# Kernel optimization log

Measured on AMD Instinct MI355X. Metric: run time of the kernel, lower is better.

## Reference

```python
import jax, jax.numpy as jnp
import numpy as np

B, T, E_DIM, H, J, V = 32, 1000, 512, 512, 512, 1024
BLANK = 0

def setup_inputs() -> dict:
    key = jax.random.key(0)
    ks = jax.random.split(key, 8)
    s = lambda k, shp, sc: jax.random.normal(k, shp, jnp.float32) * sc
    return {
        "encoder_output": jax.random.normal(ks[0], (B, T, E_DIM), jnp.float32),
        "embed": s(ks[1], (V, H), 0.02),
        "W_ih": s(ks[2], (H, 4 * H), 0.05),
        "W_hh": s(ks[3], (H, 4 * H), 0.05),
        "b_lstm": jnp.zeros((4 * H,), jnp.float32),
        "W_enc": s(ks[4], (E_DIM, J), 0.05),
        "W_dec": s(ks[5], (H, J), 0.05),
        "b_joint": jnp.zeros((J,), jnp.float32),
        "W_out": s(ks[6], (J, V), 0.05),
    }

def _lstm_step(tok, h, c, embed, W_ih, W_hh, b):
    # prediction network: embedding lookup + single-layer LSTM cell
    x = embed[tok]                                   # [B, H]
    gates = x @ W_ih + h @ W_hh + b                  # [B, 4H]
    i, f, g, o = jnp.split(gates, 4, axis=-1)
    c_new = jax.nn.sigmoid(f) * c + jax.nn.sigmoid(i) * jnp.tanh(g)
    h_new = jax.nn.sigmoid(o) * jnp.tanh(c_new)
    return h_new, c_new

def reference(encoder_output, embed, W_ih, W_hh, b_lstm, W_enc, W_dec, b_joint, W_out):
    # transducer_greedy_decode (beam_size <= 1 path), vectorized over batch,
    # sequential over encoder time steps via lax.scan.
    Bv = encoder_output.shape[0]
    h0 = jnp.zeros((Bv, H), encoder_output.dtype)
    c0 = jnp.zeros((Bv, H), encoder_output.dtype)
    tok0 = jnp.full((Bv,), BLANK, jnp.int32)
    # initial decoder call on blank token with zero hidden
    out_PN0, c1 = _lstm_step(tok0, h0, c0, embed, W_ih, W_hh, b_lstm)
    # precompute encoder projection of the joint (same math, one big GEMM)
    enc_proj = encoder_output @ W_enc                # [B, T, J]

    def step(carry, enc_t):
        out_PN, h, c, score = carry
        logits = jnp.tanh(enc_t + out_PN @ W_dec + b_joint) @ W_out   # [B, V]
        logp = jax.nn.log_softmax(logits, axis=-1)
        lp = jnp.max(logp, axis=-1)                  # best log-prob
        pos = jnp.argmax(logp, axis=-1)              # best token
        emit = pos != BLANK                          # hypotheses to update
        h_new, c_new = _lstm_step(pos.astype(jnp.int32), h, c, embed, W_ih, W_hh, b_lstm)
        m = emit[:, None]
        out_PN = jnp.where(m, h_new, out_PN)
        h = jnp.where(m, h_new, h)
        c = jnp.where(m, c_new, c)
        score = score + jnp.where(emit, lp, 0.0)
        tok = jnp.where(emit, pos, BLANK)            # BLANK marks 'no emission'
        return (out_PN, h, c, score), tok

    init = (out_PN0, out_PN0, c1, jnp.zeros((Bv,), encoder_output.dtype))
    (_, _, _, scores), toks = jax.lax.scan(step, init, jnp.swapaxes(enc_proj, 0, 1))
    predictions = toks.T                             # [B, T], BLANK = no emission
    mean_exp_score = jnp.exp(scores).mean()
    return predictions, scores, mean_exp_score
```

## Files before the change

### kernel.cpp

```cpp
#include <hip/hip_runtime.h>
#include <math.h>

#define BB 32
#define TT 1000
#define HH 512
#define JJ 512
#define VV 1024
#define G4 2048
#define NB 128
#define NT 1024

#define RLX __ATOMIC_RELAXED
#define AGT __HIP_MEMORY_SCOPE_AGENT

__device__ __align__(16) float g_encp[(size_t)TT * JJ * BB];
__device__ __align__(16) float g_E[(size_t)VV * G4];
__device__ __align__(16) float g_h[HH * BB];
__device__ __align__(16) float g_c[BB * HH];
__device__ __align__(16) float g_joint[JJ * BB];
__device__ __align__(16) float g_hW[BB * G4];
__device__ float g_pm[BB * NB];
__device__ float g_ps[BB * NB];
__device__ int   g_pa[BB * NB];
__device__ float g_score[BB];
__device__ int g_arr[3][NB];

__global__ __launch_bounds__(256) void k_encproj(const float* __restrict__ enc,
                                                 const float* __restrict__ Wenc) {
    __shared__ __align__(16) float x[BB * 512];
    const int t = blockIdx.x;
    for (int i = threadIdx.x; i < BB * 128; i += 256) {
        const int b = i >> 7, k4 = i & 127;
        *reinterpret_cast<float4*>(x + b * 512 + k4 * 4) =
            *reinterpret_cast<const float4*>(enc + ((size_t)(b * TT + t)) * 512 + k4 * 4);
    }
    __syncthreads();
    const int j = threadIdx.x;
    float acc0[BB], acc1[BB];
#pragma unroll
    for (int b = 0; b < BB; ++b) { acc0[b] = 0.f; acc1[b] = 0.f; }
    for (int k4 = 0; k4 < 128; ++k4) {
        const int k = k4 * 4;
        float w0[4], w1[4];
#pragma unroll
        for (int i = 0; i < 4; ++i) {
            w0[i] = Wenc[(size_t)(k + i) * JJ + j];
            w1[i] = Wenc[(size_t)(k + i) * JJ + j + 256];
        }
#pragma unroll
        for (int b = 0; b < BB; ++b) {
            const float4 xv = *reinterpret_cast<const float4*>(x + b * 512 + k);
            acc0[b] += xv.x * w0[0] + xv.y * w0[1] + xv.z * w0[2] + xv.w * w0[3];
            acc1[b] += xv.x * w1[0] + xv.y * w1[1] + xv.z * w1[2] + xv.w * w1[3];
        }
    }
    float* outt = g_encp + (size_t)t * JJ * BB;
#pragma unroll
    for (int b = 0; b < BB; ++b) {
        outt[j * BB + b]         = acc0[b];
        outt[(j + 256) * BB + b] = acc1[b];
    }
}

__global__ __launch_bounds__(256) void k_embproj(const float* __restrict__ emb,
                                                 const float* __restrict__ Wih) {
    __shared__ __align__(16) float x[BB * 512];
    const int v0 = (blockIdx.x >> 2) * 32;
    const int g0 = (blockIdx.x & 3) * 512;
    for (int i = threadIdx.x; i < BB * 128; i += 256) {
        const int b = i >> 7, k4 = i & 127;
        *reinterpret_cast<float4*>(x + b * 512 + k4 * 4) =
            *reinterpret_cast<const float4*>(emb + (size_t)(v0 + b) * 512 + k4 * 4);
    }
    __syncthreads();
    const int j = g0 + threadIdx.x;
    float acc0[BB], acc1[BB];
#pragma unroll
    for (int b = 0; b < BB; ++b) { acc0[b] = 0.f; acc1[b] = 0.f; }
    for (int k4 = 0; k4 < 128; ++k4) {
        const int k = k4 * 4;
        float w0[4], w1[4];
#pragma unroll
        for (int i = 0; i < 4; ++i) {
            w0[i] = Wih[(size_t)(k + i) * G4 + j];
            w1[i] = Wih[(size_t)(k + i) * G4 + j + 256];
        }
#pragma unroll
        for (int b = 0; b < BB; ++b) {
            const float4 xv = *reinterpret_cast<const float4*>(x + b * 512 + k);
            acc0[b] += xv.x * w0[0] + xv.y * w0[1] + xv.z * w0[2] + xv.w * w0[3];
            acc1[b] += xv.x * w1[0] + xv.y * w1[1] + xv.z * w1[2] + xv.w * w1[3];
        }
    }
#pragma unroll
    for (int b = 0; b < BB; ++b) {
        g_E[(size_t)(v0 + b) * G4 + j]       = acc0[b];
        g_E[(size_t)(v0 + b) * G4 + j + 256] = acc1[b];
    }
}

__global__ void k_init(const float* __restrict__ bl) {
    const int k = threadIdx.x;
    const float ig = g_E[k]        + bl[k];
    const float gg = g_E[1024 + k] + bl[1024 + k];
    const float og = g_E[1536 + k] + bl[1536 + k];
    const float si = 1.f / (1.f + expf(-ig));
    const float so = 1.f / (1.f + expf(-og));
    const float c1 = si * tanhf(gg);
    const float h1 = so * tanhf(c1);
    for (int b = 0; b < BB; ++b) {
        g_h[k * BB + b] = h1;
        g_c[b * HH + k] = c1;
    }
    if (k < BB) g_score[k] = 0.f;
    if (k < 3 * NB) ((int*)g_arr)[k] = 0;
}

template<int KN>
__device__ __forceinline__ void mv4(const float* __restrict__ w_lds, const int wpad,
                                    const int c0, const int k0,
                                    const float* __restrict__ x_lds,
                                    const int ks, const int b4, float acc[4][4]) {
#pragma unroll
    for (int c = 0; c < 4; ++c)
#pragma unroll
        for (int r = 0; r < 4; ++r) acc[c][r] = 0.f;
#pragma unroll 8
    for (int i = 0; i < KN; ++i) {
        const int k = k0 + i * 8 + ks;
        const float4 xv = *reinterpret_cast<const float4*>(x_lds + k * 32 + b4 * 4);
        const float4 wv = *reinterpret_cast<const float4*>(w_lds + k * wpad + c0);
        acc[0][0] += wv.x * xv.x; acc[0][1] += wv.x * xv.y; acc[0][2] += wv.x * xv.z; acc[0][3] += wv.x * xv.w;
        acc[1][0] += wv.y * xv.x; acc[1][1] += wv.y * xv.y; acc[1][2] += wv.y * xv.z; acc[1][3] += wv.y * xv.w;
        acc[2][0] += wv.z * xv.x; acc[2][1] += wv.z * xv.y; acc[2][2] += wv.z * xv.z; acc[2][3] += wv.z * xv.w;
        acc[3][0] += wv.w * xv.x; acc[3][1] += wv.w * xv.y; acc[3][2] += wv.w * xv.z; acc[3][3] += wv.w * xv.w;
    }
#pragma unroll
    for (int off = 8; off <= 32; off <<= 1)
#pragma unroll
        for (int c = 0; c < 4; ++c)
#pragma unroll
            for (int r = 0; r < 4; ++r) acc[c][r] += __shfl_xor(acc[c][r], off, 64);
}

__global__ __launch_bounds__(NT) void k_loop(const float* __restrict__ Wdec,
                                             const float* __restrict__ Wout,
                                             const float* __restrict__ Whh,
                                             const float* __restrict__ bj,
                                             const float* __restrict__ bl,
                                             float* __restrict__ out) {
    __shared__ __align__(16) float x_lds[512 * 32];
    __shared__ __align__(16) float wab_lds[512 * 20];
    __shared__ __align__(16) float wout_lds[512 * 12];
    __shared__ float part_lds[560];
    __shared__ float logit_lds[8 * 33];
    __shared__ float red_m[2], red_s[2];
    __shared__ int   red_a[2];
    __shared__ int   red_bar[2];
    __shared__ int   bar_done;

    const int blk = blockIdx.x, tid = threadIdx.x;
    const int wv = tid >> 6, lane = tid & 63, ks = lane >> 3, b4 = lane & 7;
    const int row = blk >> 2, qs = blk & 3;

    for (int i = tid; i < 512 * 20; i += NT) {
        const int k = i / 20, c = i - k * 20;
        wab_lds[i] = (c < 16) ? Whh[(size_t)k * G4 + blk * 16 + c]
                              : Wdec[(size_t)k * JJ + blk * 4 + (c - 16)];
    }
    for (int i = tid; i < 512 * 12; i += NT) {
        const int k = i / 12, c = i - k * 12;
        wout_lds[i] = (c < 8) ? Wout[(size_t)k * VV + blk * 8 + c] : 0.f;
    }
    float bjr[4];
#pragma unroll
    for (int c = 0; c < 4; ++c) bjr[c] = bj[blk * 4 + c];
    __syncthreads();

    float acc[4][4];
    for (int t = 0; t < TT; ++t) {
        const int tp1 = t + 1;
        {
            float v[16];
#pragma unroll
            for (int p = 0; p < 16; ++p)
                v[p] = __hip_atomic_load(&g_h[tid + p * 1024], RLX, AGT);
#pragma unroll
            for (int p = 0; p < 16; ++p) x_lds[tid + p * 1024] = v[p];
        }
        float encr[4];
        if (wv == 8 && lane < 32) {
            const float* ep = g_encp + (size_t)t * JJ * BB + (size_t)blk * 4 * BB;
#pragma unroll
            for (int c = 0; c < 4; ++c) encr[c] = ep[c * BB + lane];
        }
        __syncthreads();
        if (wv < 4) {
            mv4<64>(wab_lds, 20, wv * 4, 0, x_lds, ks, b4, acc);
            if (ks == 0) {
#pragma unroll
                for (int c = 0; c < 4; ++c)
#pragma unroll
                    for (int j = 0; j < 4; ++j)
                        __hip_atomic_store(&g_hW[(size_t)(b4 * 4 + j) * G4 + blk * 16 + wv * 4 + c],
                                           acc[c][j], RLX, AGT);
            }
        } else if (wv < 8) {
            mv4<16>(wab_lds, 20, 16, (wv - 4) * 128, x_lds, ks, b4, acc);
            if (ks == 0) {
#pragma unroll
                for (int c = 0; c < 4; ++c)
#pragma unroll
                    for (int j = 0; j < 4; ++j)
                        part_lds[(wv - 4) * 136 + c * 33 + b4 * 4 + j] = acc[c][j];
            }
        }
        __syncthreads();
        if (wv == 8 && lane < 32) {
            const int b = lane;
#pragma unroll
            for (int c = 0; c < 4; ++c) {
                const float u = part_lds[c * 33 + b] + part_lds[136 + c * 33 + b]
                              + part_lds[272 + c * 33 + b] + part_lds[408 + c * 33 + b]
                              + encr[c] + bjr[c];
                __hip_atomic_store(&g_joint[(blk * 4 + c) * BB + b], tanhf(u), RLX, AGT);
            }
        }
        __syncthreads();
        if (tid == 0) __hip_atomic_store(&g_arr[0][blk], tp1, RLX, AGT);
        for (;;) {
            int m = 0x7fffffff;
            if (tid < NB) m = __hip_atomic_load(&g_arr[0][tid], RLX, AGT);
#pragma unroll
            for (int off = 32; off; off >>= 1) m = min(m, __shfl_xor(m, off, 64));
            if (lane == 0 && wv < 2) red_bar[wv] = m;
            __syncthreads();
            if (tid == 0) bar_done = (min(red_bar[0], red_bar[1]) >= tp1);
            __syncthreads();
            if (bar_done) break;
            __builtin_amdgcn_s_sleep(1);
        }

        {
            float v[16];
#pragma unroll
            for (int p = 0; p < 16; ++p)
                v[p] = __hip_atomic_load(&g_joint[tid + p * 1024], RLX, AGT);
#pragma unroll
            for (int p = 0; p < 16; ++p) x_lds[tid + p * 1024] = v[p];
        }
        __syncthreads();
        if (wv < 4) {
            const int tile = wv & 1, kh = wv >> 1;
            mv4<32>(wout_lds, 12, tile * 4, kh * 256, x_lds, ks, b4, acc);
            if (kh == 1 && ks == 0) {
#pragma unroll
                for (int c = 0; c < 4; ++c)
#pragma unroll
                    for (int j = 0; j < 4; ++j)
                        part_lds[tile * 160 + c * 33 + b4 * 4 + j] = acc[c][j];
            }
        }
        __syncthreads();
        if (wv < 2 && ks == 0) {
#pragma unroll
            for (int c = 0; c < 4; ++c)
#pragma unroll
                for (int j = 0; j < 4; ++j)
                    logit_lds[(wv * 4 + c) * 33 + b4 * 4 + j] =
                        acc[c][j] + part_lds[wv * 160 + c * 33 + b4 * 4 + j];
        }
        __syncthreads();
        if (wv == 0 && lane < BB) {
            const int b = lane;
            float m = -1e30f; int a = 0;
#pragma unroll
            for (int c = 0; c < 8; ++c) {
                const float l = logit_lds[c * 33 + b];
                if (l > m) { m = l; a = blk * 8 + c; }
            }
            float s = 0.f;
#pragma unroll
            for (int c = 0; c < 8; ++c) s += expf(logit_lds[c * 33 + b] - m);
            __hip_atomic_store(&g_pm[b * NB + blk], m, RLX, AGT);
            __hip_atomic_store(&g_pa[b * NB + blk], a, RLX, AGT);
            __hip_atomic_store(&g_ps[b * NB + blk], s, RLX, AGT);
        }
        __syncthreads();
        if (tid == 0) __hip_atomic_store(&g_arr[1][blk], tp1, RLX, AGT);
        for (;;) {
            int m = 0x7fffffff;
            if (tid < NB) m = __hip_atomic_load(&g_arr[1][tid], RLX, AGT);
#pragma unroll
            for (int off = 32; off; off >>= 1) m = min(m, __shfl_xor(m, off, 64));
            if (lane == 0 && wv < 2) red_bar[wv] = m;
            __syncthreads();
            if (tid == 0) bar_done = (min(red_bar[0], red_bar[1]) >= tp1);
            __syncthreads();
            if (bar_done) break;
            __builtin_amdgcn_s_sleep(1);
        }

        {
            float m0 = -1e30f, s0 = 0.f; int a0 = 1 << 30;
            if (tid < NB) {
                m0 = __hip_atomic_load(&g_pm[row * NB + tid], RLX, AGT);
                a0 = __hip_atomic_load(&g_pa[row * NB + tid], RLX, AGT);
                s0 = __hip_atomic_load(&g_ps[row * NB + tid], RLX, AGT);
            }
            float m = m0; int a = a0;
#pragma unroll
            for (int off = 32; off; off >>= 1) {
                const float om = __shfl_xor(m, off, 64);
                const int   oa = __shfl_xor(a, off, 64);
                if (om > m || (om == m && oa < a)) { m = om; a = oa; }
            }
            if (lane == 0 && wv < 2) { red_m[wv] = m; red_a[wv] = a; }
            __syncthreads();
            float M; int P;
            {
                const float ma = red_m[0], mb = red_m[1];
                const int aa = red_a[0], ab = red_a[1];
                if (mb > ma || (mb == ma && ab < aa)) { M = mb; P = ab; }
                else { M = ma; P = aa; }
            }
            float e = (tid < NB) ? s0 * expf(m0 - M) : 0.f;
#pragma unroll
            for (int off = 32; off; off >>= 1) e += __shfl_xor(e, off, 64);
            if (lane == 0 && wv < 2) red_s[wv] = e;
            __syncthreads();
            if (qs == 0 && tid == 0) {
                out[row * TT + t] = (float)P;
                if (P != 0) g_score[row] += -logf(red_s[0] + red_s[1]);
            }
            if (P != 0 && tid < 128) {
                const int k = qs * 128 + tid;
                const float* Ep = g_E + (size_t)P * G4;
                const float hw0 = __hip_atomic_load(&g_hW[(size_t)row * G4 + k],        RLX, AGT);
                const float hw1 = __hip_atomic_load(&g_hW[(size_t)row * G4 + 512 + k],  RLX, AGT);
                const float hw2 = __hip_atomic_load(&g_hW[(size_t)row * G4 + 1024 + k], RLX, AGT);
                const float hw3 = __hip_atomic_load(&g_hW[(size_t)row * G4 + 1536 + k], RLX, AGT);
                const float i_g = Ep[k]        + hw0 + bl[k];
                const float f_g = Ep[512 + k]  + hw1 + bl[512 + k];
                const float g_g = Ep[1024 + k] + hw2 + bl[1024 + k];
                const float o_g = Ep[1536 + k] + hw3 + bl[1536 + k];
                const float si = 1.f / (1.f + expf(-i_g));
                const float sf = 1.f / (1.f + expf(-f_g));
                const float so = 1.f / (1.f + expf(-o_g));
                const float cn = sf * g_c[row * HH + k] + si * tanhf(g_g);
                const float hn = so * tanhf(cn);
                g_c[row * HH + k] = cn;
                __hip_atomic_store(&g_h[k * BB + row], hn, RLX, AGT);
            }
        }
        __syncthreads();
        if (tid == 0) __hip_atomic_store(&g_arr[2][blk], tp1, RLX, AGT);
        for (;;) {
            int m = 0x7fffffff;
            if (tid < NB) m = __hip_atomic_load(&g_arr[2][tid], RLX, AGT);
#pragma unroll
            for (int off = 32; off; off >>= 1) m = min(m, __shfl_xor(m, off, 64));
            if (lane == 0 && wv < 2) red_bar[wv] = m;
            __syncthreads();
            if (tid == 0) bar_done = (min(red_bar[0], red_bar[1]) >= tp1);
            __syncthreads();
            if (bar_done) break;
            __builtin_amdgcn_s_sleep(1);
        }
    }
}

__global__ void k_final(float* __restrict__ out) {
    const int b = threadIdx.x;
    float e = 0.f;
    if (b < BB) {
        const float sc = g_score[b];
        out[BB * TT + b] = sc;
        e = expf(sc);
    }
#pragma unroll
    for (int off = 32; off; off >>= 1) e += __shfl_xor(e, off, 64);
    if (b == 0) out[BB * TT + BB] = e / (float)BB;
}

extern "C" void kernel_launch(void* const* d_in, const int* in_sizes, int n_in,
                              void* d_out, int out_size, void* d_ws, size_t ws_size,
                              hipStream_t stream) {
    const float* enc  = (const float*)d_in[0];
    const float* emb  = (const float*)d_in[1];
    const float* Wih  = (const float*)d_in[2];
    const float* Whh  = (const float*)d_in[3];
    const float* bl   = (const float*)d_in[4];
    const float* Wenc = (const float*)d_in[5];
    const float* Wdec = (const float*)d_in[6];
    const float* bj   = (const float*)d_in[7];
    const float* Wout = (const float*)d_in[8];
    float* out = (float*)d_out;

    hipLaunchKernelGGL(k_encproj, dim3(TT), dim3(256), 0, stream, enc, Wenc);
    hipLaunchKernelGGL(k_embproj, dim3(128), dim3(256), 0, stream, emb, Wih);
    hipLaunchKernelGGL(k_init, dim3(1), dim3(512), 0, stream, bl);

    void* args[] = { (void*)&Wdec, (void*)&Wout, (void*)&Whh,
                     (void*)&bj, (void*)&bl, (void*)&out };
    hipLaunchCooperativeKernel((const void*)k_loop, dim3(NB), dim3(NT), args, 0, stream);

    hipLaunchKernelGGL(k_final, dim3(1), dim3(64), 0, stream, out);
}
```

Measured before the change: 31.77 ms.

## Replace grid barriers with single-wave tag polling and defer the h barrier

The three per-step grid barriers become per-block tags, each padded to its own 16-byte slot. Only one wavefront polls them, spinning without sleep and without block-wide syncs inside the loop. The third barrier, after the LSTM update, now moves to the start of the next step, so the encoder-projection prefetch overlaps the wait. This is meant to cut barrier latency on the serial 1000-step critical path, at the cost of busier spinning that puts more load on the memory system.

```diff
diff --git a/kernel.cpp b/kernel.cpp
--- a/kernel.cpp
+++ b/kernel.cpp
@@ -23,7 +23,9 @@
 __device__ float g_ps[BB * NB];
 __device__ int   g_pa[BB * NB];
 __device__ float g_score[BB];
-__device__ int g_arr[3][NB];
+__device__ int g_tagJ[NB * 4];
+__device__ int g_tagS[NB * 4];
+__device__ int g_tagH[NB * 4];
 
 __global__ __launch_bounds__(256) void k_encproj(const float* __restrict__ enc,
                                                  const float* __restrict__ Wenc) {
@@ -113,7 +115,7 @@
         g_c[b * HH + k] = c1;
     }
     if (k < BB) g_score[k] = 0.f;
-    if (k < 3 * NB) ((int*)g_arr)[k] = 0;
+    g_tagJ[k] = 0; g_tagS[k] = 0; g_tagH[k] = 0;
 }
 
 template<int KN>
@@ -141,6 +143,20 @@
         for (int c = 0; c < 4; ++c)
 #pragma unroll
             for (int r = 0; r < 4; ++r) acc[c][r] += __shfl_xor(acc[c][r], off, 64);
+}
+
+__device__ __forceinline__ void tag_poll(const int* tags, int thr, int wv, int lane) {
+    if (wv == 0) {
+        for (;;) {
+            int a = __hip_atomic_load(&tags[lane * 4], RLX, AGT);
+            int b = __hip_atomic_load(&tags[(lane + 64) * 4], RLX, AGT);
+            int m = min(a, b);
+#pragma unroll
+            for (int off = 32; off; off >>= 1) m = min(m, __shfl_xor(m, off, 64));
+            if (m >= thr) break;
+        }
+    }
+    __syncthreads();
 }
 
 __global__ __launch_bounds__(NT) void k_loop(const float* __restrict__ Wdec,
@@ -156,8 +172,6 @@
     __shared__ float logit_lds[8 * 33];
     __shared__ float red_m[2], red_s[2];
     __shared__ int   red_a[2];
-    __shared__ int   red_bar[2];
-    __shared__ int   bar_done;
 
     const int blk = blockIdx.x, tid = threadIdx.x;
     const int wv = tid >> 6, lane = tid & 63, ks = lane >> 3, b4 = lane & 7;
@@ -180,19 +194,21 @@
     float acc[4][4];
     for (int t = 0; t < TT; ++t) {
         const int tp1 = t + 1;
-        {
-            float v[16];
-#pragma unroll
-            for (int p = 0; p < 16; ++p)
-                v[p] = __hip_atomic_load(&g_h[tid + p * 1024], RLX, AGT);
-#pragma unroll
-            for (int p = 0; p < 16; ++p) x_lds[tid + p * 1024] = v[p];
-        }
+
         float encr[4];
         if (wv == 8 && lane < 32) {
             const float* ep = g_encp + (size_t)t * JJ * BB + (size_t)blk * 4 * BB;
 #pragma unroll
             for (int c = 0; c < 4; ++c) encr[c] = ep[c * BB + lane];
+        }
+        tag_poll(g_tagH, t, wv, lane);
+        {
+            float v[16];
+#pragma unroll
+            for (int p = 0; p < 16; ++p)
+                v[p] = __hip_atomic_load(&g_h[tid + p * 1024], RLX, AGT);
+#pragma unroll
+            for (int p = 0; p < 16; ++p) x_lds[tid + p * 1024] = v[p];
         }
         __syncthreads();
         if (wv < 4) {
@@ -227,20 +243,9 @@
             }
         }
         __syncthreads();
-        if (tid == 0) __hip_atomic_store(&g_arr[0][blk], tp1, RLX, AGT);
-        for (;;) {
-            int m = 0x7fffffff;
-            if (tid < NB) m = __hip_atomic_load(&g_arr[0][tid], RLX, AGT);
-#pragma unroll
-            for (int off = 32; off; off >>= 1) m = min(m, __shfl_xor(m, off, 64));
-            if (lane == 0 && wv < 2) red_bar[wv] = m;
-            __syncthreads();
-            if (tid == 0) bar_done = (min(red_bar[0], red_bar[1]) >= tp1);
-            __syncthreads();
-            if (bar_done) break;
-            __builtin_amdgcn_s_sleep(1);
-        }
-
+        if (tid == 0) __hip_atomic_store(&g_tagJ[blk * 4], tp1, RLX, AGT);
+
+        tag_poll(g_tagJ, tp1, wv, lane);
         {
             float v[16];
 #pragma unroll
@@ -287,20 +292,9 @@
             __hip_atomic_store(&g_ps[b * NB + blk], s, RLX, AGT);
         }
         __syncthreads();
-        if (tid == 0) __hip_atomic_store(&g_arr[1][blk], tp1, RLX, AGT);
-        for (;;) {
-            int m = 0x7fffffff;
-            if (tid < NB) m = __hip_atomic_load(&g_arr[1][tid], RLX, AGT);
-#pragma unroll
-            for (int off = 32; off; off >>= 1) m = min(m, __shfl_xor(m, off, 64));
-            if (lane == 0 && wv < 2) red_bar[wv] = m;
-            __syncthreads();
-            if (tid == 0) bar_done = (min(red_bar[0], red_bar[1]) >= tp1);
-            __syncthreads();
-            if (bar_done) break;
-            __builtin_amdgcn_s_sleep(1);
-        }
-
+        if (tid == 0) __hip_atomic_store(&g_tagS[blk * 4], tp1, RLX, AGT);
+
+        tag_poll(g_tagS, tp1, wv, lane);
         {
             float m0 = -1e30f, s0 = 0.f; int a0 = 1 << 30;
             if (tid < NB) {
@@ -354,19 +348,7 @@
             }
         }
         __syncthreads();
-        if (tid == 0) __hip_atomic_store(&g_arr[2][blk], tp1, RLX, AGT);
-        for (;;) {
-            int m = 0x7fffffff;
-            if (tid < NB) m = __hip_atomic_load(&g_arr[2][tid], RLX, AGT);
-#pragma unroll
-            for (int off = 32; off; off >>= 1) m = min(m, __shfl_xor(m, off, 64));
-            if (lane == 0 && wv < 2) red_bar[wv] = m;
-            __syncthreads();
-            if (tid == 0) bar_done = (min(red_bar[0], red_bar[1]) >= tp1);
-            __syncthreads();
-            if (bar_done) break;
-            __builtin_amdgcn_s_sleep(1);
-        }
+        if (tid == 0) __hip_atomic_store(&g_tagH[blk * 4], tp1, RLX, AGT);
     }
 }
 
```

After: 26.06 ms. 1.22x faster.
